# Performance work log

Hardware: AMD Instinct MI355X
Metric: run time of the kernel (lower is better)

The kernel has to match this reference:

```python
import jax, jax.numpy as jnp
import numpy as np

B_, T_, TS, DE, H, LD, OD = 16, 4096, 64, 128, 256, 512, 10
RMIN, RMAX, MAXPH = 0.9, 0.999, 6.283
EPS = 1e-5
NBLK = 6


def setup_inputs() -> dict:
    key = jax.random.key(0)
    ks = jax.random.split(key, 14)
    x = jax.random.normal(ks[0], (B_, T_, TS), jnp.float32)
    # LRU ring init (Orvieto et al.)
    u1 = jax.random.uniform(ks[1], (NBLK, H))
    u2 = jax.random.uniform(ks[2], (NBLK, H))
    nu_log = jnp.log(-0.5 * jnp.log(u1 * (RMAX**2 - RMIN**2) + RMIN**2))
    theta_log = jnp.log(MAXPH * u2)
    B_re = jax.random.normal(ks[3], (NBLK, H, DE)) / np.sqrt(2 * DE)
    B_im = jax.random.normal(ks[4], (NBLK, H, DE)) / np.sqrt(2 * DE)
    C_re = jax.random.normal(ks[5], (NBLK, DE, H)) / np.sqrt(H)
    C_im = jax.random.normal(ks[6], (NBLK, DE, H)) / np.sqrt(H)
    D_lru = jax.random.normal(ks[7], (NBLK, DE))
    W1 = jax.random.normal(ks[8], (NBLK, DE, LD)) / np.sqrt(DE)
    b1 = jnp.zeros((NBLK, LD))
    W2 = jax.random.normal(ks[9], (NBLK, LD // 2, DE)) / np.sqrt(LD // 2)
    b2 = jnp.zeros((NBLK, DE))
    bn_scale = jnp.ones((NBLK, DE))
    bn_bias = jnp.zeros((NBLK, DE))
    W_enc = jax.random.normal(ks[10], (TS, DE)) / np.sqrt(TS)
    b_enc = jnp.zeros((DE,))
    W_out = jax.random.normal(ks[11], (DE, OD)) / np.sqrt(DE)
    b_out = jnp.zeros((OD,))
    return dict(x=x, nu_log=nu_log, theta_log=theta_log, B_re=B_re, B_im=B_im,
                C_re=C_re, C_im=C_im, D_lru=D_lru, W1=W1, b1=b1, W2=W2, b2=b2,
                bn_scale=bn_scale, bn_bias=bn_bias, W_enc=W_enc, b_enc=b_enc,
                W_out=W_out, b_out=b_out)


def _lru(u, nu_log_i, theta_log_i, Bre, Bim, Cre, Cim, Dv):
    # u: [B,T,DE] float. Diagonal complex linear recurrence via associative scan.
    lam = jnp.exp(-jnp.exp(nu_log_i) + 1j * jnp.exp(theta_log_i))        # [H]
    gamma = jnp.sqrt(jnp.clip(1.0 - jnp.abs(lam) ** 2, 1e-8, None))      # [H]
    Bc = (Bre + 1j * Bim) * gamma[:, None]                               # [H,DE]
    Bu = jnp.einsum('btd,hd->bth', u.astype(jnp.complex64), Bc)          # [B,T,H]
    lam_b = jnp.broadcast_to(lam, Bu.shape)

    def binop(a, b):
        return (a[0] * b[0], a[1] * b[0] + b[1])

    _, h = jax.lax.associative_scan(binop, (lam_b, Bu), axis=1)          # [B,T,H]
    y = jnp.einsum('bth,dh->btd', h, Cre + 1j * Cim).real + u * Dv
    return y


def _bn(x, scale, bias):
    # training-mode batchnorm over (batch, time) with feature axis last
    m = x.mean(axis=(0, 1))
    v = x.var(axis=(0, 1))
    return (x - m) * jax.lax.rsqrt(v + EPS) * scale + bias


def reference(x, nu_log, theta_log, B_re, B_im, C_re, C_im, D_lru,
              W1, b1, W2, b2, bn_scale, bn_bias, W_enc, b_enc, W_out, b_out):
    h = x @ W_enc + b_enc                       # [B,T,DE]
    y = h
    for i in range(NBLK):
        z = _bn(h, bn_scale[i], bn_bias[i])
        z = _lru(z, nu_log[i], theta_log[i], B_re[i], B_im[i], C_re[i], C_im[i], D_lru[i])
        z = z @ W1[i] + b1[i]                   # [B,T,LD]
        a, b = jnp.split(z, 2, axis=-1)
        z = a * jax.nn.sigmoid(b)               # GLU
        z = z @ W2[i] + b2[i]                   # [B,T,DE]
        h = z + y                               # residual to encoder output
    pooled = h.mean(axis=1)                     # pool=True: mean over tokens
    return pooled @ W_out + b_out               # [B,OD]
```

## Files before the change

kernel.cpp:

```cpp
#include <hip/hip_runtime.h>
#include <hip/hip_fp16.h>

#define BB 16
#define TT 4096
#define TSZ 64
#define DE 128
#define HH 256
#define LDIM 512
#define ODIM 10
#define NBLKS 6
#define EPSF 1e-5f
#define NC32 128
#define NROWS (BB*TT)

typedef _Float16 f16x8 __attribute__((ext_vector_type(8)));
typedef _Float16 f16x4 __attribute__((ext_vector_type(4)));
typedef float f32x4 __attribute__((ext_vector_type(4)));
#define MFMA16(a,b,c) __builtin_amdgcn_mfma_f32_16x16x32_f16((a),(b),(c),0,0,0)

enum : size_t {
  HOFF_BG = 0,
  HOFF_WC = HOFF_BG + (size_t)NBLKS*512*128,
  HOFF_W1 = HOFF_WC + (size_t)NBLKS*128*512,
  HOFF_W2 = HOFF_W1 + (size_t)NBLKS*512*128,
  HOFF_WE = HOFF_W2 + (size_t)NBLKS*128*256,
  HTOT_HALFS = HOFF_WE + 128*64
};

enum : size_t {
  WOFF_Y     = 0,
  WOFF_H     = WOFF_Y + (size_t)NROWS*DE/2,
  WOFF_W16   = WOFF_H + (size_t)NROWS*DE/2,
  WOFF_LAM   = WOFF_W16 + (HTOT_HALFS+1)/2,
  WOFF_LAML  = WOFF_LAM + (size_t)NBLKS*HH*2,
  WOFF_SL    = WOFF_LAML + (size_t)NBLKS*HH*2,
  WOFF_CARRY = WOFF_SL + (size_t)BB*NC32*HH*2,
  WOFF_STATS = WOFF_CARRY + (size_t)BB*NC32*HH*2,
  WOFF_POOL  = WOFF_STATS + (size_t)(NBLKS+1)*2*DE,
  WOFF_BU    = WOFF_POOL + (size_t)BB*DE,
  WS_FLOATS  = WOFF_BU + (size_t)BB*NC32*512*32/2
};

__global__ __launch_bounds__(256) void k_prep(
    const float* __restrict__ nu_log, const float* __restrict__ theta_log,
    const float* __restrict__ B_re, const float* __restrict__ B_im,
    const float* __restrict__ C_re, const float* __restrict__ C_im,
    const float* __restrict__ W1g, const float* __restrict__ W2g,
    const float* __restrict__ Wenc, float* __restrict__ ws)
{
  const int i = blockIdx.x, h = threadIdx.x;
  __half* w16 = (__half*)(ws + WOFF_W16);
  const float nu  = expf(nu_log[i*HH+h]);
  const float th  = expf(theta_log[i*HH+h]);
  const float mod = expf(-nu);
  const float lr = mod*cosf(th), li = mod*sinf(th);
  const float gamma = sqrtf(fmaxf(1.0f - mod*mod, 1e-8f));
  ws[WOFF_LAM + ((size_t)i*HH+h)*2+0] = lr;
  ws[WOFF_LAM + ((size_t)i*HH+h)*2+1] = li;
  {
    float ar = lr, ai = li;
    #pragma unroll
    for (int q = 0; q < 5; q++) { float nr=ar*ar-ai*ai, ni=2.0f*ar*ai; ar=nr; ai=ni; }
    ws[WOFF_LAML + ((size_t)i*HH+h)*2+0] = ar;
    ws[WOFF_LAML + ((size_t)i*HH+h)*2+1] = ai;
  }
  {
    __half* bg = w16 + HOFF_BG + (size_t)i*512*128;
    const float* bre = B_re + ((size_t)i*HH+h)*DE;
    const float* bim = B_im + ((size_t)i*HH+h)*DE;
    for (int d = 0; d < DE; d++) {
      bg[(size_t)h*128 + d]       = __float2half(bre[d]*gamma);
      bg[(size_t)(256+h)*128 + d] = __float2half(bim[d]*gamma);
    }
  }
  {
    __half* wc = w16 + HOFF_WC + (size_t)i*128*512;
    const float* cre = C_re + (size_t)i*DE*HH;
    const float* cim = C_im + (size_t)i*DE*HH;
    for (int d = 0; d < DE; d++) {
      wc[(size_t)d*512 + 2*h]     = __float2half( cre[(size_t)d*HH + h]);
      wc[(size_t)d*512 + 2*h + 1] = __float2half(-cim[(size_t)d*HH + h]);
    }
  }
  {
    __half* w1t = w16 + HOFF_W1 + (size_t)i*512*128;
    for (int d = 0; d < DE; d++) {
      w1t[(size_t)h*128 + d]       = __float2half(W1g[((size_t)i*DE + d)*LDIM + h]);
      w1t[(size_t)(256+h)*128 + d] = __float2half(W1g[((size_t)i*DE + d)*LDIM + 256 + h]);
    }
  }
  if (h < 128) {
    __half* w2t = w16 + HOFF_W2 + (size_t)i*128*256;
    for (int g = 0; g < 256; g++)
      w2t[(size_t)h*256 + g] = __float2half(W2g[((size_t)i*256 + g)*DE + h]);
  }
  if (i == 0 && h < 128) {
    __half* wet = w16 + HOFF_WE;
    for (int k = 0; k < TSZ; k++)
      wet[(size_t)h*TSZ + k] = __float2half(Wenc[(size_t)k*DE + h]);
  }
}

__global__ __launch_bounds__(512) void k_enc(
    const float* __restrict__ x, const float* __restrict__ benc, float* __restrict__ ws)
{
  __shared__ __half XT[64*72];
  __shared__ __half YS[64*136];
  const int tid = threadIdx.x, w = tid >> 6, l = tid & 63;
  const size_t row0 = (size_t)blockIdx.x * 64;
  {
    const float4* xg = (const float4*)(x + row0*TSZ);
    for (int idx = tid; idx < 1024; idx += 512) {
      float4 v = xg[idx];
      const int r = idx >> 4, c4 = (idx & 15)*4;
      *(__half2*)&XT[r*72 + c4]     = __half2{__float2half(v.x), __float2half(v.y)};
      *(__half2*)&XT[r*72 + c4 + 2] = __half2{__float2half(v.z), __float2half(v.w)};
    }
  }
  __syncthreads();
  const __half* wet = (const __half*)(ws + WOFF_W16) + HOFF_WE;
  const int n0 = w*16;
  f32x4 acc[4];
  #pragma unroll
  for (int mt = 0; mt < 4; mt++) acc[mt] = (f32x4)(0.0f);
  #pragma unroll
  for (int k0 = 0; k0 < 64; k0 += 32) {
    f16x8 bf = *(const f16x8*)&wet[(size_t)(n0 + (l&15))*64 + k0 + (l>>4)*8];
    #pragma unroll
    for (int mt = 0; mt < 4; mt++) {
      f16x8 af = *(const f16x8*)&XT[(mt*16 + (l&15))*72 + k0 + (l>>4)*8];
      acc[mt] = MFMA16(af, bf, acc[mt]);
    }
  }
  const int d = n0 + (l&15);
  const float be = benc[d];
  float s = 0.0f, ss = 0.0f;
  #pragma unroll
  for (int mt = 0; mt < 4; mt++)
    #pragma unroll
    for (int j = 0; j < 4; j++) {
      const int t = mt*16 + (l>>4)*4 + j;
      const float v = acc[mt][j] + be;
      YS[t*136 + d] = __float2half(v);
      s += v; ss += v*v;
    }
  s  += __shfl_xor(s, 16);  s  += __shfl_xor(s, 32);
  ss += __shfl_xor(ss, 16); ss += __shfl_xor(ss, 32);
  if (l < 16) {
    atomicAdd(ws + WOFF_STATS + d, s);
    atomicAdd(ws + WOFF_STATS + DE + d, ss);
  }
  __syncthreads();
  __half* y = (__half*)(ws + WOFF_Y);
  const int row = tid >> 3, d0 = (tid & 7)*16;
  *(f16x8*)&y[(row0+row)*DE + d0]     = *(const f16x8*)&YS[row*136 + d0];
  *(f16x8*)&y[(row0+row)*DE + d0 + 8] = *(const f16x8*)&YS[row*136 + d0 + 8];
}

__global__ __launch_bounds__(512, 4) void k_A(
    const __half* __restrict__ hin, float* __restrict__ ws,
    const float* __restrict__ bnsg, const float* __restrict__ bnbg, int iblk)
{
  __shared__ __half U[32*136];
  __shared__ __half BU[32*520];
  __shared__ float AC[256];
  const int tid = threadIdx.x, w = tid >> 6, l = tid & 63, q = l >> 4, r = l & 15;
  const int b = blockIdx.y, cbg = blockIdx.x;
  const int h = tid & 255;
  if (tid < 128) {
    const float inv = 1.0f / (float)NROWS;
    const float s  = ws[WOFF_STATS + ((size_t)iblk*2+0)*DE + tid];
    const float sq = ws[WOFF_STATS + ((size_t)iblk*2+1)*DE + tid];
    const float mean = s*inv;
    const float var  = sq*inv - mean*mean;
    const float a = rsqrtf(var + EPSF) * bnsg[iblk*DE + tid];
    AC[tid]       = a;
    AC[128 + tid] = bnbg[iblk*DE + tid] - mean*a;
  }
  const __half* BG = (const __half*)(ws + WOFF_W16) + HOFF_BG + (size_t)iblk*512*128;
  const int n0 = w*64;
  const float lr = ws[WOFF_LAM + ((size_t)iblk*HH+h)*2+0];
  const float li = ws[WOFF_LAM + ((size_t)iblk*HH+h)*2+1];
  f16x8 bg4[4][4];
  #pragma unroll
  for (int nt = 0; nt < 4; nt++)
    #pragma unroll
    for (int k = 0; k < 4; k++)
      bg4[nt][k] = *(const f16x8*)&BG[(size_t)(n0 + nt*16 + r)*128 + k*32 + q*8];
  __half* bug = (__half*)(ws + WOFF_BU);
  __syncthreads();

  for (int it = 0; it < 4; it++) {
    const int cb = cbg*4 + it;
    const int row0 = b*TT + cb*32;
    {
      const int row = tid >> 4, d0 = (tid & 15)*8;
      f16x8 hv = *(const f16x8*)(hin + (size_t)(row0+row)*DE + d0);
      f16x8 uv;
      #pragma unroll
      for (int j = 0; j < 8; j++)
        uv[j] = (_Float16)((float)hv[j]*AC[d0+j] + AC[128+d0+j]);
      *(f16x8*)&U[row*136 + d0] = uv;
    }
    __syncthreads();
    {
      f32x4 acc[2][4];
      #pragma unroll
      for (int mt = 0; mt < 2; mt++)
        #pragma unroll
        for (int nt = 0; nt < 4; nt++) acc[mt][nt] = (f32x4)(0.0f);
      #pragma unroll
      for (int k = 0; k < 4; k++) {
        f16x8 af0 = *(const f16x8*)&U[(r)*136      + k*32 + q*8];
        f16x8 af1 = *(const f16x8*)&U[(16 + r)*136 + k*32 + q*8];
        #pragma unroll
        for (int nt = 0; nt < 4; nt++) {
          acc[0][nt] = MFMA16(af0, bg4[nt][k], acc[0][nt]);
          acc[1][nt] = MFMA16(af1, bg4[nt][k], acc[1][nt]);
        }
      }
      #pragma unroll
      for (int mt = 0; mt < 2; mt++)
        #pragma unroll
        for (int nt = 0; nt < 4; nt++) {
          f16x4 pk;
          #pragma unroll
          for (int j = 0; j < 4; j++) {
            pk[j] = (_Float16)acc[mt][nt][j];
            BU[(mt*16 + q*4 + j)*520 + n0 + nt*16 + r] = __float2half(acc[mt][nt][j]);
          }
          const int hc = n0 + nt*16 + r;
          *(f16x4*)(bug + (((size_t)(b*NC32 + cb)*512 + hc)*32 + mt*16 + q*4)) = pk;
        }
    }
    __syncthreads();
    if (tid < 256) {
      float sr = 0.0f, si = 0.0f;
      #pragma unroll
      for (int t = 0; t < 32; t++) {
        const float br = (float)BU[t*520 + h];
        const float bi = (float)BU[t*520 + 256 + h];
        const float nr = lr*sr - li*si + br;
        const float ni = lr*si + li*sr + bi;
        sr = nr; si = ni;
      }
      *((float2*)(ws + WOFF_SL) + ((size_t)b*NC32 + cb)*HH + h) = float2{sr, si};
    }
    __syncthreads();
  }
}

__global__ void k_carry(float* __restrict__ ws, int i)
{
  const int b = blockIdx.x >> 2;
  const int h = (blockIdx.x & 3)*64 + threadIdx.x;
  const float Lr = ws[WOFF_LAML + ((size_t)i*HH+h)*2+0];
  const float Li = ws[WOFF_LAML + ((size_t)i*HH+h)*2+1];
  float2* C = (float2*)(ws + WOFF_CARRY) + (size_t)b*NC32*HH + h;
  const float2* S = (const float2*)(ws + WOFF_SL) + (size_t)b*NC32*HH + h;
  float sr = 0.0f, si = 0.0f;
  C[0] = float2{0.0f, 0.0f};
  for (int c0 = 0; c0 < 120; c0 += 8) {
    float2 sl[8];
    #pragma unroll
    for (int j = 0; j < 8; j++) sl[j] = S[(size_t)(c0+j)*HH];
    #pragma unroll
    for (int j = 0; j < 8; j++) {
      const float nr = Lr*sr - Li*si + sl[j].x;
      const float ni = Lr*si + Li*sr + sl[j].y;
      sr = nr; si = ni;
      C[(size_t)(c0+j+1)*HH] = float2{sr, si};
    }
  }
  {
    float2 sl[7];
    #pragma unroll
    for (int j = 0; j < 7; j++) sl[j] = S[(size_t)(120+j)*HH];
    #pragma unroll
    for (int j = 0; j < 7; j++) {
      const float nr = Lr*sr - Li*si + sl[j].x;
      const float ni = Lr*si + Li*sr + sl[j].y;
      sr = nr; si = ni;
      C[(size_t)(121+j)*HH] = float2{sr, si};
    }
  }
}

__global__ __launch_bounds__(512, 4) void k_BC(
    const __half* __restrict__ hin, float* __restrict__ ws,
    const float* __restrict__ bnsg, const float* __restrict__ bnbg,
    const float* __restrict__ b1g, const float* __restrict__ b2g,
    const float* __restrict__ Dvg, int iblk, int islast)
{
  __shared__ __half U[32*136];
  __shared__ __half HT[32*520];
  __shared__ __half YL[32*136];
  __shared__ __half YR[32*136];
  __shared__ float AC[256];
  __shared__ float DVs[128];
  const int tid = threadIdx.x, w = tid >> 6, l = tid & 63, q = l >> 4, r = l & 15;
  const int b = blockIdx.y, cbg = blockIdx.x;
  const __half* w16 = (const __half*)(ws + WOFF_W16);
  const int d = w*16 + r;
  const int h = tid & 255;

  if (tid < 128) {
    const float inv = 1.0f / (float)NROWS;
    const float s  = ws[WOFF_STATS + ((size_t)iblk*2+0)*DE + tid];
    const float sq = ws[WOFF_STATS + ((size_t)iblk*2+1)*DE + tid];
    const float mean = s*inv;
    const float var  = sq*inv - mean*mean;
    const float a = rsqrtf(var + EPSF) * bnsg[iblk*DE + tid];
    AC[tid]       = a;
    AC[128 + tid] = bnbg[iblk*DE + tid] - mean*a;
    DVs[tid] = Dvg[iblk*DE + tid];
  }

  const float lr = ws[WOFF_LAM + ((size_t)iblk*HH+h)*2+0];
  const float li = ws[WOFF_LAM + ((size_t)iblk*HH+h)*2+1];
  float b1a[2], b1b[2];
  #pragma unroll
  for (int nt = 0; nt < 2; nt++) {
    const int ca = w*32 + nt*16 + r;
    b1a[nt] = b1g[(size_t)iblk*LDIM + ca];
    b1b[nt] = b1g[(size_t)iblk*LDIM + 256 + ca];
  }
  const float bb2 = b2g[(size_t)iblk*DE + d];
  const __half* WC  = w16 + HOFF_WC + (size_t)iblk*128*512;
  const __half* W1T = w16 + HOFF_W1 + (size_t)iblk*512*128;
  const __half* W2T = w16 + HOFF_W2 + (size_t)iblk*128*256;
  const __half* bug = (const __half*)(ws + WOFF_BU);
  const __half* yh = (const __half*)(ws + WOFF_Y);
  __half* hh = (__half*)(ws + WOFF_H);
  float s_acc = 0.0f, ss_acc = 0.0f;
  __syncthreads();

  for (int it = 0; it < 4; it++) {
    const int cb = cbg*4 + it;
    const int row0 = b*TT + cb*32;

    {
      const int row = tid >> 4, d0 = (tid & 15)*8;
      f16x8 hv  = *(const f16x8*)(hin + (size_t)(row0+row)*DE + d0);
      f16x8 yv8 = *(const f16x8*)(yh  + (size_t)(row0+row)*DE + d0);
      f16x8 uv;
      #pragma unroll
      for (int j = 0; j < 8; j++)
        uv[j] = (_Float16)((float)hv[j]*AC[d0+j] + AC[128+d0+j]);
      *(f16x8*)&U[row*136 + d0]  = uv;
      *(f16x8*)&YR[row*136 + d0] = yv8;
    }
    if (tid < 256) {
      const __half* bu = bug + ((size_t)(b*NC32 + cb)*512)*32;
      f16x8 bre[4], bim[4];
      #pragma unroll
      for (int k = 0; k < 4; k++) {
        bre[k] = *(const f16x8*)(bu + (size_t)h*32 + k*8);
        bim[k] = *(const f16x8*)(bu + (size_t)(256+h)*32 + k*8);
      }
      const float2 carry = *((const float2*)(ws + WOFF_CARRY) + ((size_t)b*NC32 + cb)*HH + h);
      float sr = carry.x, si = carry.y;
      #pragma unroll
      for (int t = 0; t < 32; t++) {
        const float br = (float)bre[t>>3][t&7];
        const float bi = (float)bim[t>>3][t&7];
        const float nr = lr*sr - li*si + br;
        const float ni = lr*si + li*sr + bi;
        sr = nr; si = ni;
        *(__half2*)&HT[t*520 + 2*h] = __half2{__float2half(sr), __float2half(si)};
      }
    }
    __syncthreads();

    {
      f16x8 wc[16];
      #pragma unroll
      for (int k = 0; k < 16; k++)
        wc[k] = *(const f16x8*)&WC[(size_t)d*512 + k*32 + q*8];
      f32x4 a0 = (f32x4)(0.0f), a1 = (f32x4)(0.0f);
      #pragma unroll
      for (int k = 0; k < 16; k++) {
        f16x8 af0 = *(const f16x8*)&HT[(r)*520      + k*32 + q*8];
        f16x8 af1 = *(const f16x8*)&HT[(16 + r)*520 + k*32 + q*8];
        a0 = MFMA16(af0, wc[k], a0);
        a1 = MFMA16(af1, wc[k], a1);
      }
      const float dv = DVs[d];
      #pragma unroll
      for (int mt = 0; mt < 2; mt++)
        #pragma unroll
        for (int j = 0; j < 4; j++) {
          const int t = mt*16 + q*4 + j;
          const float u = (float)U[t*136 + d];
          YL[t*136 + d] = __float2half((mt ? a1[j] : a0[j]) + u*dv);
        }
    }
    __syncthreads();

    {
      #pragma unroll
      for (int nt = 0; nt < 2; nt++) {
        const int ca = w*32 + nt*16 + r;
        f16x8 wa[4], wb[4];
        #pragma unroll
        for (int k = 0; k < 4; k++) {
          wa[k] = *(const f16x8*)&W1T[(size_t)ca*128 + k*32 + q*8];
          wb[k] = *(const f16x8*)&W1T[(size_t)(256+ca)*128 + k*32 + q*8];
        }
        f32x4 aa0 = (f32x4)(0.0f), aa1 = (f32x4)(0.0f);
        f32x4 ab0 = (f32x4)(0.0f), ab1 = (f32x4)(0.0f);
        #pragma unroll
        for (int k = 0; k < 4; k++) {
          f16x8 af0 = *(const f16x8*)&YL[(r)*136      + k*32 + q*8];
          f16x8 af1 = *(const f16x8*)&YL[(16 + r)*136 + k*32 + q*8];
          aa0 = MFMA16(af0, wa[k], aa0);
          aa1 = MFMA16(af1, wa[k], aa1);
          ab0 = MFMA16(af0, wb[k], ab0);
          ab1 = MFMA16(af1, wb[k], ab1);
        }
        #pragma unroll
        for (int mt = 0; mt < 2; mt++)
          #pragma unroll
          for (int j = 0; j < 4; j++) {
            const int t = mt*16 + q*4 + j;
            const float av = (mt ? aa1[j] : aa0[j]) + b1a[nt];
            const float bv = (mt ? ab1[j] : ab0[j]) + b1b[nt];
            HT[t*520 + ca] = __float2half(av / (1.0f + __expf(-bv)));
          }
      }
    }
    __syncthreads();

    {
      f16x8 w2f[8];
      #pragma unroll
      for (int k = 0; k < 8; k++)
        w2f[k] = *(const f16x8*)&W2T[(size_t)d*256 + k*32 + q*8];
      f32x4 a0 = (f32x4)(0.0f), a1 = (f32x4)(0.0f);
      #pragma unroll
      for (int k = 0; k < 8; k++) {
        f16x8 af0 = *(const f16x8*)&HT[(r)*520      + k*32 + q*8];
        f16x8 af1 = *(const f16x8*)&HT[(16 + r)*520 + k*32 + q*8];
        a0 = MFMA16(af0, w2f[k], a0);
        a1 = MFMA16(af1, w2f[k], a1);
      }
      #pragma unroll
      for (int mt = 0; mt < 2; mt++)
        #pragma unroll
        for (int j = 0; j < 4; j++) {
          const int t = mt*16 + q*4 + j;
          const float v = (mt ? a1[j] : a0[j]) + bb2 + (float)YR[t*136 + d];
          YR[t*136 + d] = __float2half(v);
          s_acc += v; ss_acc += v*v;
        }
    }
    __syncthreads();

    {
      const int row = tid >> 4, d0 = (tid & 15)*8;
      *(f16x8*)(hh + (size_t)(row0+row)*DE + d0) = *(const f16x8*)&YR[row*136 + d0];
    }
    __syncthreads();
  }

  s_acc  += __shfl_xor(s_acc, 16);  s_acc  += __shfl_xor(s_acc, 32);
  ss_acc += __shfl_xor(ss_acc, 16); ss_acc += __shfl_xor(ss_acc, 32);
  if (l < 16) {
    atomicAdd(ws + WOFF_STATS + (size_t)((iblk+1)*2 + 0)*DE + d, s_acc);
    atomicAdd(ws + WOFF_STATS + (size_t)((iblk+1)*2 + 1)*DE + d, ss_acc);
    if (islast) atomicAdd(ws + WOFF_POOL + (size_t)b*DE + d, s_acc);
  }
}

__global__ void k_out(const float* __restrict__ Wout, const float* __restrict__ bout,
                      const float* __restrict__ ws, float* __restrict__ out)
{
  const int tid = threadIdx.x;
  if (tid < BB*ODIM) {
    const int b = tid / ODIM, o = tid % ODIM;
    float acc = bout[o];
    const float* p = ws + WOFF_POOL + (size_t)b*DE;
    const float invT = 1.0f / (float)TT;
    for (int d = 0; d < DE; d++) acc += p[d]*invT*Wout[d*ODIM + o];
    out[tid] = acc;
  }
}

extern "C" void kernel_launch(void* const* d_in, const int* in_sizes, int n_in,
                              void* d_out, int out_size, void* d_ws, size_t ws_size,
                              hipStream_t stream)
{
  const float* x   = (const float*)d_in[0];
  const float* nu  = (const float*)d_in[1];
  const float* th  = (const float*)d_in[2];
  const float* Bre = (const float*)d_in[3];
  const float* Bim = (const float*)d_in[4];
  const float* Cre = (const float*)d_in[5];
  const float* Cim = (const float*)d_in[6];
  const float* Dv  = (const float*)d_in[7];
  const float* W1  = (const float*)d_in[8];
  const float* b1  = (const float*)d_in[9];
  const float* W2  = (const float*)d_in[10];
  const float* b2  = (const float*)d_in[11];
  const float* bns = (const float*)d_in[12];
  const float* bnb = (const float*)d_in[13];
  const float* We  = (const float*)d_in[14];
  const float* be  = (const float*)d_in[15];
  const float* Wo  = (const float*)d_in[16];
  const float* bo  = (const float*)d_in[17];
  float* ws = (float*)d_ws;
  float* out = (float*)d_out;

  hipMemsetAsync(ws + WOFF_STATS, 0,
                 (size_t)(((NBLKS+1)*2*DE) + BB*DE)*sizeof(float), stream);

  k_prep<<<NBLKS, 256, 0, stream>>>(nu, th, Bre, Bim, Cre, Cim, W1, W2, We, ws);
  k_enc<<<NROWS/64, 512, 0, stream>>>(x, be, ws);

  const __half* Yh = (const __half*)(ws + WOFF_Y);
  const __half* Hh = (const __half*)(ws + WOFF_H);
  for (int i = 0; i < NBLKS; i++) {
    const __half* hin = (i == 0) ? Yh : Hh;
    k_A    <<<dim3(32, BB), 512, 0, stream>>>(hin, ws, bns, bnb, i);
    k_carry<<<64, 64, 0, stream>>>(ws, i);
    k_BC   <<<dim3(32, BB), 512, 0, stream>>>(hin, ws, bns, bnb, b1, b2, Dv, i,
                                              (i == NBLKS-1) ? 1 : 0);
  }
  k_out<<<1, 256, 0, stream>>>(Wo, bo, ws, out);
}
```

Before: 901.0 us.

## Store local chunk scan states and apply carry via precomputed lambda powers

The first pass now runs the in-chunk complex scan and writes the zero-carry local states to global memory, replacing the raw Bu values. The second pass no longer reruns the 32-step serial recurrence. It adds the carry contribution using precomputed tables of lambda^t, reconstructing all states in parallel across every thread. The C-projection weight layout is split into separate real and imaginary halves, and the YR shared buffer is dropped by reusing U. The intent is to remove a serial recurrence from the heavier second kernel and cut LDS use, in exchange for storing half-precision powers and local states, which may reduce accuracy.

```diff
diff --git a/kernel.cpp b/kernel.cpp
--- a/kernel.cpp
+++ b/kernel.cpp
@@ -14,7 +14,6 @@
 #define NROWS (BB*TT)
 
 typedef _Float16 f16x8 __attribute__((ext_vector_type(8)));
-typedef _Float16 f16x4 __attribute__((ext_vector_type(4)));
 typedef float f32x4 __attribute__((ext_vector_type(4)));
 #define MFMA16(a,b,c) __builtin_amdgcn_mfma_f32_16x16x32_f16((a),(b),(c),0,0,0)
 
@@ -24,7 +23,9 @@
   HOFF_W1 = HOFF_WC + (size_t)NBLKS*128*512,
   HOFF_W2 = HOFF_W1 + (size_t)NBLKS*512*128,
   HOFF_WE = HOFF_W2 + (size_t)NBLKS*128*256,
-  HTOT_HALFS = HOFF_WE + 128*64
+  HOFF_PA = HOFF_WE + 128*64,
+  HOFF_PB = HOFF_PA + (size_t)NBLKS*32*512,
+  HTOT_HALFS = HOFF_PB + (size_t)NBLKS*32*512
 };
 
 enum : size_t {
@@ -37,8 +38,8 @@
   WOFF_CARRY = WOFF_SL + (size_t)BB*NC32*HH*2,
   WOFF_STATS = WOFF_CARRY + (size_t)BB*NC32*HH*2,
   WOFF_POOL  = WOFF_STATS + (size_t)(NBLKS+1)*2*DE,
-  WOFF_BU    = WOFF_POOL + (size_t)BB*DE,
-  WS_FLOATS  = WOFF_BU + (size_t)BB*NC32*512*32/2
+  WOFF_HL    = WOFF_POOL + (size_t)BB*DE,
+  WS_FLOATS  = WOFF_HL + (size_t)BB*NC32*32*512/2
 };
 
 __global__ __launch_bounds__(256) void k_prep(
@@ -65,6 +66,19 @@
     ws[WOFF_LAML + ((size_t)i*HH+h)*2+1] = ai;
   }
   {
+    __half* PA = w16 + HOFF_PA + (size_t)i*32*512;
+    __half* PB = w16 + HOFF_PB + (size_t)i*32*512;
+    float pr = lr, pi = li;
+    for (int t = 0; t < 32; t++) {
+      PA[(size_t)t*512 + h]       = __float2half(pr);
+      PA[(size_t)t*512 + 256 + h] = __float2half(pi);
+      PB[(size_t)t*512 + h]       = __float2half(-pi);
+      PB[(size_t)t*512 + 256 + h] = __float2half(pr);
+      const float nr = pr*lr - pi*li, ni = pr*li + pi*lr;
+      pr = nr; pi = ni;
+    }
+  }
+  {
     __half* bg = w16 + HOFF_BG + (size_t)i*512*128;
     const float* bre = B_re + ((size_t)i*HH+h)*DE;
     const float* bim = B_im + ((size_t)i*HH+h)*DE;
@@ -78,8 +92,8 @@
     const float* cre = C_re + (size_t)i*DE*HH;
     const float* cim = C_im + (size_t)i*DE*HH;
     for (int d = 0; d < DE; d++) {
-      wc[(size_t)d*512 + 2*h]     = __float2half( cre[(size_t)d*HH + h]);
-      wc[(size_t)d*512 + 2*h + 1] = __float2half(-cim[(size_t)d*HH + h]);
+      wc[(size_t)d*512 + h]       = __float2half( cre[(size_t)d*HH + h]);
+      wc[(size_t)d*512 + 256 + h] = __float2half(-cim[(size_t)d*HH + h]);
     }
   }
   {
@@ -162,7 +176,7 @@
     const float* __restrict__ bnsg, const float* __restrict__ bnbg, int iblk)
 {
   __shared__ __half U[32*136];
-  __shared__ __half BU[32*520];
+  __shared__ __half BU[32*536];
   __shared__ float AC[256];
   const int tid = threadIdx.x, w = tid >> 6, l = tid & 63, q = l >> 4, r = l & 15;
   const int b = blockIdx.y, cbg = blockIdx.x;
@@ -187,7 +201,7 @@
     #pragma unroll
     for (int k = 0; k < 4; k++)
       bg4[nt][k] = *(const f16x8*)&BG[(size_t)(n0 + nt*16 + r)*128 + k*32 + q*8];
-  __half* bug = (__half*)(ws + WOFF_BU);
+  __half* hlg = (__half*)(ws + WOFF_HL);
   __syncthreads();
 
   for (int it = 0; it < 4; it++) {
@@ -222,29 +236,35 @@
       #pragma unroll
       for (int mt = 0; mt < 2; mt++)
         #pragma unroll
-        for (int nt = 0; nt < 4; nt++) {
-          f16x4 pk;
+        for (int nt = 0; nt < 4; nt++)
           #pragma unroll
-          for (int j = 0; j < 4; j++) {
-            pk[j] = (_Float16)acc[mt][nt][j];
-            BU[(mt*16 + q*4 + j)*520 + n0 + nt*16 + r] = __float2half(acc[mt][nt][j]);
-          }
-          const int hc = n0 + nt*16 + r;
-          *(f16x4*)(bug + (((size_t)(b*NC32 + cb)*512 + hc)*32 + mt*16 + q*4)) = pk;
-        }
+          for (int j = 0; j < 4; j++)
+            BU[(mt*16 + q*4 + j)*536 + n0 + nt*16 + r] = __float2half(acc[mt][nt][j]);
     }
     __syncthreads();
     if (tid < 256) {
       float sr = 0.0f, si = 0.0f;
       #pragma unroll
       for (int t = 0; t < 32; t++) {
-        const float br = (float)BU[t*520 + h];
-        const float bi = (float)BU[t*520 + 256 + h];
+        const float br = (float)BU[t*536 + h];
+        const float bi = (float)BU[t*536 + 256 + h];
         const float nr = lr*sr - li*si + br;
         const float ni = lr*si + li*sr + bi;
         sr = nr; si = ni;
+        BU[t*536 + h]       = __float2half(sr);
+        BU[t*536 + 256 + h] = __float2half(si);
       }
       *((float2*)(ws + WOFF_SL) + ((size_t)b*NC32 + cb)*HH + h) = float2{sr, si};
+    }
+    __syncthreads();
+    {
+      __half* dst = hlg + ((size_t)(b*NC32 + cb)*32)*512;
+      #pragma unroll
+      for (int g = 0; g < 4; g++) {
+        const int idx = tid + g*512;
+        const int row = idx >> 6, col = (idx & 63)*8;
+        *(f16x8*)(dst + (size_t)row*512 + col) = *(const f16x8*)&BU[row*536 + col];
+      }
     }
     __syncthreads();
   }
@@ -295,14 +315,12 @@
   __shared__ __half U[32*136];
   __shared__ __half HT[32*520];
   __shared__ __half YL[32*136];
-  __shared__ __half YR[32*136];
   __shared__ float AC[256];
   __shared__ float DVs[128];
   const int tid = threadIdx.x, w = tid >> 6, l = tid & 63, q = l >> 4, r = l & 15;
   const int b = blockIdx.y, cbg = blockIdx.x;
   const __half* w16 = (const __half*)(ws + WOFF_W16);
   const int d = w*16 + r;
-  const int h = tid & 255;
 
   if (tid < 128) {
     const float inv = 1.0f / (float)NROWS;
@@ -316,20 +334,21 @@
     DVs[tid] = Dvg[iblk*DE + tid];
   }
 
-  const float lr = ws[WOFF_LAM + ((size_t)iblk*HH+h)*2+0];
-  const float li = ws[WOFF_LAM + ((size_t)iblk*HH+h)*2+1];
-  float b1a[2], b1b[2];
+  const __half* PA = w16 + HOFF_PA + (size_t)iblk*32*512;
+  const __half* PB = w16 + HOFF_PB + (size_t)iblk*32*512;
+  f16x8 pa[4], pb[4];
   #pragma unroll
-  for (int nt = 0; nt < 2; nt++) {
-    const int ca = w*32 + nt*16 + r;
-    b1a[nt] = b1g[(size_t)iblk*LDIM + ca];
-    b1b[nt] = b1g[(size_t)iblk*LDIM + 256 + ca];
+  for (int g = 0; g < 4; g++) {
+    const int idx = tid + g*512;
+    const int row = idx >> 6, col = (idx & 63)*8;
+    pa[g] = *(const f16x8*)&PA[(size_t)row*512 + col];
+    pb[g] = *(const f16x8*)&PB[(size_t)row*512 + col];
   }
   const float bb2 = b2g[(size_t)iblk*DE + d];
   const __half* WC  = w16 + HOFF_WC + (size_t)iblk*128*512;
   const __half* W1T = w16 + HOFF_W1 + (size_t)iblk*512*128;
   const __half* W2T = w16 + HOFF_W2 + (size_t)iblk*128*256;
-  const __half* bug = (const __half*)(ws + WOFF_BU);
+  const __half* hlg = (const __half*)(ws + WOFF_HL);
   const __half* yh = (const __half*)(ws + WOFF_Y);
   __half* hh = (__half*)(ws + WOFF_H);
   float s_acc = 0.0f, ss_acc = 0.0f;
@@ -341,49 +360,52 @@
 
     {
       const int row = tid >> 4, d0 = (tid & 15)*8;
-      f16x8 hv  = *(const f16x8*)(hin + (size_t)(row0+row)*DE + d0);
-      f16x8 yv8 = *(const f16x8*)(yh  + (size_t)(row0+row)*DE + d0);
+      f16x8 hv = *(const f16x8*)(hin + (size_t)(row0+row)*DE + d0);
       f16x8 uv;
       #pragma unroll
       for (int j = 0; j < 8; j++)
         uv[j] = (_Float16)((float)hv[j]*AC[d0+j] + AC[128+d0+j]);
-      *(f16x8*)&U[row*136 + d0]  = uv;
-      *(f16x8*)&YR[row*136 + d0] = yv8;
-    }
-    if (tid < 256) {
-      const __half* bu = bug + ((size_t)(b*NC32 + cb)*512)*32;
-      f16x8 bre[4], bim[4];
-      #pragma unroll
-      for (int k = 0; k < 4; k++) {
-        bre[k] = *(const f16x8*)(bu + (size_t)h*32 + k*8);
-        bim[k] = *(const f16x8*)(bu + (size_t)(256+h)*32 + k*8);
-      }
-      const float2 carry = *((const float2*)(ws + WOFF_CARRY) + ((size_t)b*NC32 + cb)*HH + h);
-      float sr = carry.x, si = carry.y;
-      #pragma unroll
-      for (int t = 0; t < 32; t++) {
-        const float br = (float)bre[t>>3][t&7];
-        const float bi = (float)bim[t>>3][t&7];
-        const float nr = lr*sr - li*si + br;
-        const float ni = lr*si + li*sr + bi;
-        sr = nr; si = ni;
-        *(__half2*)&HT[t*520 + 2*h] = __half2{__float2half(sr), __float2half(si)};
-      }
-    }
-    __syncthreads();
-
-    {
-      f16x8 wc[16];
-      #pragma unroll
-      for (int k = 0; k < 16; k++)
-        wc[k] = *(const f16x8*)&WC[(size_t)d*512 + k*32 + q*8];
+      *(f16x8*)&U[row*136 + d0] = uv;
+    }
+    {
+      const __half* src = hlg + ((size_t)(b*NC32 + cb)*32)*512;
+      const float* cg = ws + WOFF_CARRY + ((size_t)b*NC32 + cb)*HH*2;
+      #pragma unroll
+      for (int g = 0; g < 4; g++) {
+        const int idx = tid + g*512;
+        const int row = idx >> 6, col = (idx & 63)*8;
+        const int h0 = col & 255;
+        f16x8 lv = *(const f16x8*)(src + (size_t)row*512 + col);
+        float4 c0 = *(const float4*)(cg + h0*2);
+        float4 c1 = *(const float4*)(cg + h0*2 + 4);
+        float4 c2 = *(const float4*)(cg + h0*2 + 8);
+        float4 c3 = *(const float4*)(cg + h0*2 + 12);
+        const float cr[8] = {c0.x, c0.z, c1.x, c1.z, c2.x, c2.z, c3.x, c3.z};
+        const float ci[8] = {c0.y, c0.w, c1.y, c1.w, c2.y, c2.w, c3.y, c3.w};
+        f16x8 hv;
+        #pragma unroll
+        for (int j = 0; j < 8; j++)
+          hv[j] = (_Float16)((float)lv[j] + (float)pa[g][j]*cr[j] + (float)pb[g][j]*ci[j]);
+        *(f16x8*)&HT[row*520 + col] = hv;
+      }
+    }
+    __syncthreads();
+
+    {
       f32x4 a0 = (f32x4)(0.0f), a1 = (f32x4)(0.0f);
       #pragma unroll
-      for (int k = 0; k < 16; k++) {
-        f16x8 af0 = *(const f16x8*)&HT[(r)*520      + k*32 + q*8];
-        f16x8 af1 = *(const f16x8*)&HT[(16 + r)*520 + k*32 + q*8];
-        a0 = MFMA16(af0, wc[k], a0);
-        a1 = MFMA16(af1, wc[k], a1);
+      for (int kb = 0; kb < 2; kb++) {
+        f16x8 wc[8];
+        #pragma unroll
+        for (int k = 0; k < 8; k++)
+          wc[k] = *(const f16x8*)&WC[(size_t)d*512 + kb*256 + k*32 + q*8];
+        #pragma unroll
+        for (int k = 0; k < 8; k++) {
+          f16x8 af0 = *(const f16x8*)&HT[(r)*520      + kb*256 + k*32 + q*8];
+          f16x8 af1 = *(const f16x8*)&HT[(16 + r)*520 + kb*256 + k*32 + q*8];
+          a0 = MFMA16(af0, wc[k], a0);
+          a1 = MFMA16(af1, wc[k], a1);
+        }
       }
       const float dv = DVs[d];
       #pragma unroll
@@ -398,36 +420,40 @@
     __syncthreads();
 
     {
-      #pragma unroll
-      for (int nt = 0; nt < 2; nt++) {
-        const int ca = w*32 + nt*16 + r;
-        f16x8 wa[4], wb[4];
-        #pragma unroll
-        for (int k = 0; k < 4; k++) {
-          wa[k] = *(const f16x8*)&W1T[(size_t)ca*128 + k*32 + q*8];
-          wb[k] = *(const f16x8*)&W1T[(size_t)(256+ca)*128 + k*32 + q*8];
+      const int row = tid >> 4, d0 = (tid & 15)*8;
+      *(f16x8*)&U[row*136 + d0] = *(const f16x8*)(yh + (size_t)(row0+row)*DE + d0);
+    }
+    #pragma unroll
+    for (int nt = 0; nt < 2; nt++) {
+      const int ca = w*32 + nt*16 + r;
+      f16x8 wa[4], wb[4];
+      #pragma unroll
+      for (int k = 0; k < 4; k++) {
+        wa[k] = *(const f16x8*)&W1T[(size_t)ca*128 + k*32 + q*8];
+        wb[k] = *(const f16x8*)&W1T[(size_t)(256+ca)*128 + k*32 + q*8];
+      }
+      f32x4 aa0 = (f32x4)(0.0f), aa1 = (f32x4)(0.0f);
+      f32x4 ab0 = (f32x4)(0.0f), ab1 = (f32x4)(0.0f);
+      #pragma unroll
+      for (int k = 0; k < 4; k++) {
+        f16x8 af0 = *(const f16x8*)&YL[(r)*136      + k*32 + q*8];
+        f16x8 af1 = *(const f16x8*)&YL[(16 + r)*136 + k*32 + q*8];
+        aa0 = MFMA16(af0, wa[k], aa0);
+        aa1 = MFMA16(af1, wa[k], aa1);
+        ab0 = MFMA16(af0, wb[k], ab0);
+        ab1 = MFMA16(af1, wb[k], ab1);
+      }
+      const float b1a = b1g[(size_t)iblk*LDIM + ca];
+      const float b1b = b1g[(size_t)iblk*LDIM + 256 + ca];
+      #pragma unroll
+      for (int mt = 0; mt < 2; mt++)
+        #pragma unroll
+        for (int j = 0; j < 4; j++) {
+          const int t = mt*16 + q*4 + j;
+          const float av = (mt ? aa1[j] : aa0[j]) + b1a;
+          const float bv = (mt ? ab1[j] : ab0[j]) + b1b;
+          HT[t*520 + ca] = __float2half(av / (1.0f + __expf(-bv)));
         }
-        f32x4 aa0 = (f32x4)(0.0f), aa1 = (f32x4)(0.0f);
-        f32x4 ab0 = (f32x4)(0.0f), ab1 = (f32x4)(0.0f);
-        #pragma unroll
-        for (int k = 0; k < 4; k++) {
-          f16x8 af0 = *(const f16x8*)&YL[(r)*136      + k*32 + q*8];
-          f16x8 af1 = *(const f16x8*)&YL[(16 + r)*136 + k*32 + q*8];
-          aa0 = MFMA16(af0, wa[k], aa0);
-          aa1 = MFMA16(af1, wa[k], aa1);
-          ab0 = MFMA16(af0, wb[k], ab0);
-          ab1 = MFMA16(af1, wb[k], ab1);
-        }
-        #pragma unroll
-        for (int mt = 0; mt < 2; mt++)
-          #pragma unroll
-          for (int j = 0; j < 4; j++) {
-            const int t = mt*16 + q*4 + j;
-            const float av = (mt ? aa1[j] : aa0[j]) + b1a[nt];
-            const float bv = (mt ? ab1[j] : ab0[j]) + b1b[nt];
-            HT[t*520 + ca] = __float2half(av / (1.0f + __expf(-bv)));
-          }
-      }
     }
     __syncthreads();
 
@@ -449,8 +475,8 @@
         #pragma unroll
         for (int j = 0; j < 4; j++) {
           const int t = mt*16 + q*4 + j;
-          const float v = (mt ? a1[j] : a0[j]) + bb2 + (float)YR[t*136 + d];
-          YR[t*136 + d] = __float2half(v);
+          const float v = (mt ? a1[j] : a0[j]) + bb2 + (float)U[t*136 + d];
+          U[t*136 + d] = __float2half(v);
           s_acc += v; ss_acc += v*v;
         }
     }
@@ -458,7 +484,7 @@
 
     {
       const int row = tid >> 4, d0 = (tid & 15)*8;
-      *(f16x8*)(hh + (size_t)(row0+row)*DE + d0) = *(const f16x8*)&YR[row*136 + d0];
+      *(f16x8*)(hh + (size_t)(row0+row)*DE + d0) = *(const f16x8*)&U[row*136 + d0];
     }
     __syncthreads();
   }
```

New measurement: 1.163 ms. 29.1% more time.
